# Kernel tuning notes

Hardware: AMD Instinct MI355X
Metric: run time of the kernel (lower is better)

Reference implementation:

```python
import jax, jax.numpy as jnp
import numpy as np

NBITS = 8
NUM_HEADS = 6


def _quant(x, alpha, nbits=NBITS):
    # LSQ-style fake quantization with straight-through estimator.
    qn = -(2 ** (nbits - 1))        # -128
    qp = 2 ** (nbits - 1) - 1       # 127
    s = jnp.clip(x / alpha, qn, qp)
    s = s + jax.lax.stop_gradient(jnp.round(s) - s)  # STE round
    return s * alpha


def setup_inputs() -> dict:
    key = jax.random.key(0)
    ks = jax.random.split(key, 12)
    B, N, C = 2, 2048, 384
    x = jax.random.normal(ks[0], (B, N, C), dtype=jnp.float32)
    w_qkv = jax.random.normal(ks[1], (3 * C, C), dtype=jnp.float32) * 0.02
    w_proj = jax.random.normal(ks[2], (C, C), dtype=jnp.float32) * 0.02
    b_proj = jnp.zeros((C,), dtype=jnp.float32)

    def alpha(k, lo, hi):
        return jax.random.uniform(k, (1,), dtype=jnp.float32, minval=lo, maxval=hi)

    return {
        "x": x,
        "w_qkv": w_qkv,
        "w_proj": w_proj,
        "b_proj": b_proj,
        "a_qkv_w": alpha(ks[3], 0.001, 0.005),
        "a_qkv_a": alpha(ks[4], 0.02, 0.05),
        "a_proj_w": alpha(ks[5], 0.001, 0.005),
        "a_proj_a": alpha(ks[6], 0.02, 0.05),
        "a_q": alpha(ks[7], 0.01, 0.03),
        "a_k": alpha(ks[8], 0.01, 0.03),
        "a_v": alpha(ks[9], 0.01, 0.03),
        "a_attn": alpha(ks[10], 0.01, 0.03),
        "a_attn2": alpha(ks[11], 0.005, 0.01),
    }


def reference(x, w_qkv, w_proj, b_proj, a_qkv_w, a_qkv_a, a_proj_w, a_proj_a,
              a_q, a_k, a_v, a_attn, a_attn2):
    B, N, C = x.shape
    H = NUM_HEADS
    D = C // H
    scale = D ** (-0.5)

    # quantized qkv linear (no bias)
    qkv = _quant(x, a_qkv_a) @ _quant(w_qkv, a_qkv_w).T          # [B,N,3C]
    qkv = qkv.reshape(B, N, 3, H, D).transpose(2, 0, 3, 1, 4)    # [3,B,H,N,D]
    q, k, v = qkv[0], qkv[1], qkv[2]
    q = _quant(q, a_q)
    k = _quant(k, a_k)
    v = _quant(v, a_v)

    attn = jnp.einsum("bhnd,bhmd->bhnm", q, k) * scale           # [B,H,N,N]
    attn = _quant(attn, a_attn)
    attn = jax.nn.softmax(attn, axis=-1)
    attn = _quant(attn, a_attn2)

    out = jnp.einsum("bhnm,bhmd->bhnd", attn, v)                 # [B,H,N,D]
    out = out.transpose(0, 2, 1, 3).reshape(B, N, C)

    # quantized output projection (with bias)
    out = _quant(out, a_proj_a) @ _quant(w_proj, a_proj_w).T + b_proj
    return out
```

## Files before the change

kernel.cpp:

```cpp
#include <hip/hip_runtime.h>
#include <math.h>


typedef int i32x4 __attribute__((ext_vector_type(4)));

#define MFMA_I8(a, b, c) __builtin_amdgcn_mfma_i32_16x16x64_i8(a, b, c, 0, 0, 0)

__device__ __forceinline__ float qclip(float s) {
  return fminf(fmaxf(s, -128.0f), 127.0f);
}

__global__ __launch_bounds__(256)
void quant16(const float* __restrict__ in, signed char* __restrict__ out,
             const float* __restrict__ alpha, int n16) {
  int i = blockIdx.x * 256 + threadIdx.x;
  if (i >= n16) return;
  float a = alpha[0];
  const float4* p = (const float4*)in + 4 * (size_t)i;
  union { uint4 u; signed char c[16]; } o;
#pragma unroll
  for (int u = 0; u < 4; ++u) {
    float4 v = p[u];
    o.c[4 * u + 0] = (signed char)(int)rintf(qclip(v.x / a));
    o.c[4 * u + 1] = (signed char)(int)rintf(qclip(v.y / a));
    o.c[4 * u + 2] = (signed char)(int)rintf(qclip(v.z / a));
    o.c[4 * u + 3] = (signed char)(int)rintf(qclip(v.w / a));
  }
  *(uint4*)(out + 16 * (size_t)i) = o.u;
}

__global__ __launch_bounds__(256)
void exp_table(float* __restrict__ E2, const float* __restrict__ aattn) {
  int i = blockIdx.x * 256 + threadIdx.x;
  float a = aattn[0];
  int vm = (i >> 8) - 128;
  int s = (i & 255) - 128;
  float m = a * (float)vm;
  E2[i] = expf(a * (float)s - m);
}

__global__ __launch_bounds__(256)
void gemm_qkv(const signed char* __restrict__ A, const signed char* __restrict__ W,
              signed char* __restrict__ qws, signed char* __restrict__ kws,
              signed char* __restrict__ vwsT,
              const float* __restrict__ aa, const float* __restrict__ aw,
              const float* __restrict__ aq, const float* __restrict__ ak,
              const float* __restrict__ av) {
  const int t = threadIdx.x;
  const int w = t >> 6, lane = t & 63;
  const int lm = lane & 15, quad = lane >> 4;
  const int wm = w >> 1, wn = w & 1;
  const int m0 = blockIdx.x * 128 + wm * 64;
  const int n0 = blockIdx.y * 128 + wn * 64;
  i32x4 acc[4][4] = {};
  for (int k0 = 0; k0 < 384; k0 += 64) {
    i32x4 af[4], bf[4];
#pragma unroll
    for (int mt = 0; mt < 4; ++mt)
      af[mt] = *(const i32x4*)(A + (size_t)(m0 + mt * 16 + lm) * 384 + k0 + quad * 16);
#pragma unroll
    for (int nt = 0; nt < 4; ++nt)
      bf[nt] = *(const i32x4*)(W + (size_t)(n0 + nt * 16 + lm) * 384 + k0 + quad * 16);
#pragma unroll
    for (int mt = 0; mt < 4; ++mt)
#pragma unroll
      for (int nt = 0; nt < 4; ++nt)
        acc[mt][nt] = MFMA_I8(af[mt], bf[nt], acc[mt][nt]);
  }
  const float sAB = aa[0] * aw[0];
  const float vaq = aq[0], vak = ak[0], vav = av[0];
#pragma unroll
  for (int mt = 0; mt < 4; ++mt) {
#pragma unroll
    for (int nt = 0; nt < 4; ++nt) {
      int cg = n0 + nt * 16 + lm;
      int t3 = cg / 384;
      int rem = cg - t3 * 384;
      int h = rem >> 6, d = rem & 63;
#pragma unroll
      for (int r = 0; r < 4; ++r) {
        int m = m0 + mt * 16 + quad * 4 + r;
        int bb = m >> 11, nn = m & 2047;
        int bh = bb * 6 + h;
        float val = (float)acc[mt][nt][r] * sAB;
        if (t3 == 0) {
          qws[((size_t)(bh * 2048 + nn) << 6) + d] = (signed char)(int)rintf(qclip(val / vaq));
        } else if (t3 == 1) {
          kws[((size_t)(bh * 2048 + nn) << 6) + d] = (signed char)(int)rintf(qclip(val / vak));
        } else {
          vwsT[((size_t)((bh << 6) + d) << 11) + nn] = (signed char)(int)rintf(qclip(val / vav));
        }
      }
    }
  }
}

#define TROW 2064
__global__ __launch_bounds__(256)
void attn_fused(const signed char* __restrict__ qws, const signed char* __restrict__ kws,
                const signed char* __restrict__ vwsT, const float* __restrict__ E2,
                signed char* __restrict__ ows,
                const float* __restrict__ aq, const float* __restrict__ ak,
                const float* __restrict__ aattn, const float* __restrict__ aattn2,
                const float* __restrict__ av, const float* __restrict__ apa) {
  __shared__ signed char tileS[16 * TROW];
  __shared__ float EfS[16 * 256];
  const int t = threadIdx.x;
  const int w = t >> 6, lane = t & 63;
  const int lm = lane & 15, quad = lane >> 4;
  const int i0 = blockIdx.x * 16;
  const int bh = blockIdx.y;

  const signed char* Qb = qws + ((size_t)bh << 17);
  const signed char* Kb = kws + ((size_t)bh << 17);

  i32x4 bq = *(const i32x4*)(Qb + ((size_t)(i0 + lm) << 6) + quad * 16);
  const float sc = aq[0] * ak[0] * 0.125f;
  const float ia = aattn[0];
#pragma unroll 4
  for (int ct = 0; ct < 32; ++ct) {
    int col0 = (w << 9) + ct * 16;
    i32x4 akf = *(const i32x4*)(Kb + ((size_t)(col0 + lm) << 6) + quad * 16);
    i32x4 z = {};
    i32x4 acc = MFMA_I8(akf, bq, z);
    union { unsigned int u; signed char c[4]; } pk;
#pragma unroll
    for (int r = 0; r < 4; ++r) {
      float sv = (float)acc[r] * sc;
      pk.c[r] = (signed char)(int)rintf(qclip(sv / ia));
    }
    *(unsigned int*)(tileS + lm * TROW + col0 + quad * 4) = pk.u;
  }
  __syncthreads();

  const float a2 = aattn2[0];
  unsigned int pqpack[4];
  signed char* lut8 = (signed char*)EfS;
#pragma unroll
  for (int rr = 0; rr < 4; ++rr) {
    const int row = w * 4 + rr;
    const char4* prow = (const char4*)(tileS + row * TROW);
    char4 vals[8];
    int vmax = -129;
#pragma unroll
    for (int u = 0; u < 8; ++u) {
      vals[u] = prow[lane + (u << 6)];
      vmax = max(vmax, (int)vals[u].x);
      vmax = max(vmax, (int)vals[u].y);
      vmax = max(vmax, (int)vals[u].z);
      vmax = max(vmax, (int)vals[u].w);
    }
#pragma unroll
    for (int off = 32; off > 0; off >>= 1)
      vmax = max(vmax, __shfl_xor(vmax, off, 64));
    float4 ef = *(const float4*)(E2 + (((vmax + 128) << 8) + (lane << 2)));
    *(float4*)(EfS + (row << 8) + (lane << 2)) = ef;
    const float* Er = EfS + (row << 8) + 128;
    float l = 0.0f;
#pragma unroll
    for (int u = 0; u < 8; ++u) {
      l += Er[(int)vals[u].x];
      l += Er[(int)vals[u].y];
      l += Er[(int)vals[u].z];
      l += Er[(int)vals[u].w];
    }
#pragma unroll
    for (int off = 32; off > 0; off >>= 1)
      l += __shfl_xor(l, off, 64);
    union { unsigned int u; signed char c[4]; } pk;
    pk.c[0] = (signed char)(int)rintf(qclip(ef.x / l / a2));
    pk.c[1] = (signed char)(int)rintf(qclip(ef.y / l / a2));
    pk.c[2] = (signed char)(int)rintf(qclip(ef.z / l / a2));
    pk.c[3] = (signed char)(int)rintf(qclip(ef.w / l / a2));
    pqpack[rr] = pk.u;
  }
  __syncthreads();

#pragma unroll
  for (int rr = 0; rr < 4; ++rr)
    *(unsigned int*)(lut8 + (((w * 4 + rr) << 8) + (lane << 2))) = pqpack[rr];
  __syncthreads();

  i32x4 areg[8];
  {
    const signed char* lr = lut8 + lm * 256 + 128;
    const signed char* srow = tileS + lm * TROW + (w << 9) + quad * 16;
#pragma unroll
    for (int js = 0; js < 8; ++js) {
      union { uint4 u; signed char c[16]; } sv;
      sv.u = *(const uint4*)(srow + js * 64);
      union { i32x4 v; signed char c[16]; } dv;
#pragma unroll
      for (int b = 0; b < 16; ++b) dv.c[b] = lr[(int)sv.c[b]];
      areg[js] = dv.v;
    }
  }

  const signed char* Vb = vwsT + ((size_t)bh << 17) + (w << 9);
  i32x4 acc[4] = {};
#pragma unroll
  for (int js = 0; js < 8; ++js) {
    int j0 = js * 64;
    i32x4 bf[4];
#pragma unroll
    for (int nt = 0; nt < 4; ++nt)
      bf[nt] = *(const i32x4*)(Vb + ((size_t)(nt * 16 + lm) << 11) + j0 + quad * 16);
#pragma unroll
    for (int nt = 0; nt < 4; ++nt)
      acc[nt] = MFMA_I8(areg[js], bf[nt], acc[nt]);
  }

  int* red = (int*)tileS;
  __syncthreads();
  if (w > 0) {
    int* rw = red + (w - 1) * 1088 + lane * 17;
#pragma unroll
    for (int nt = 0; nt < 4; ++nt)
#pragma unroll
      for (int r = 0; r < 4; ++r)
        rw[nt * 4 + r] = acc[nt][r];
  }
  __syncthreads();
  if (w == 0) {
    const float so = a2 * av[0];
    const float ipa = apa[0];
    int bb = bh / 6, h = bh % 6;
#pragma unroll
    for (int nt = 0; nt < 4; ++nt) {
      int d = nt * 16 + lm;
#pragma unroll
      for (int r = 0; r < 4; ++r) {
        int s = acc[nt][r] + red[lane * 17 + nt * 4 + r]
              + red[1088 + lane * 17 + nt * 4 + r]
              + red[2176 + lane * 17 + nt * 4 + r];
        int i = i0 + quad * 4 + r;
        ows[(size_t)((bb << 11) + i) * 384 + (h << 6) + d] =
            (signed char)(int)rintf(qclip((float)s * so / ipa));
      }
    }
  }
}

__global__ __launch_bounds__(256)
void gemm_proj(const signed char* __restrict__ A, const signed char* __restrict__ W,
               const float* __restrict__ bias, float* __restrict__ out,
               const float* __restrict__ apa, const float* __restrict__ apw) {
  const int t = threadIdx.x;
  const int w = t >> 6, lane = t & 63;
  const int lm = lane & 15, quad = lane >> 4;
  const int wm = w >> 1, wn = w & 1;
  const int m0 = blockIdx.x * 64 + wm * 32;
  const int n0 = blockIdx.y * 64 + wn * 32;
  i32x4 acc[2][2] = {};
  for (int k0 = 0; k0 < 384; k0 += 64) {
    i32x4 af[2], bf[2];
#pragma unroll
    for (int mt = 0; mt < 2; ++mt)
      af[mt] = *(const i32x4*)(A + (size_t)(m0 + mt * 16 + lm) * 384 + k0 + quad * 16);
#pragma unroll
    for (int nt = 0; nt < 2; ++nt)
      bf[nt] = *(const i32x4*)(W + (size_t)(n0 + nt * 16 + lm) * 384 + k0 + quad * 16);
#pragma unroll
    for (int mt = 0; mt < 2; ++mt)
#pragma unroll
      for (int nt = 0; nt < 2; ++nt)
        acc[mt][nt] = MFMA_I8(af[mt], bf[nt], acc[mt][nt]);
  }
  const float sAB = apa[0] * apw[0];
#pragma unroll
  for (int mt = 0; mt < 2; ++mt) {
#pragma unroll
    for (int nt = 0; nt < 2; ++nt) {
      int cg = n0 + nt * 16 + lm;
#pragma unroll
      for (int r = 0; r < 4; ++r) {
        int m = m0 + mt * 16 + quad * 4 + r;
        out[(size_t)m * 384 + cg] = (float)acc[mt][nt][r] * sAB + bias[cg];
      }
    }
  }
}

extern "C" void kernel_launch(void* const* d_in, const int* in_sizes, int n_in,
                              void* d_out, int out_size, void* d_ws, size_t ws_size,
                              hipStream_t stream) {
  const float* x        = (const float*)d_in[0];
  const float* w_qkv    = (const float*)d_in[1];
  const float* w_proj   = (const float*)d_in[2];
  const float* b_proj   = (const float*)d_in[3];
  const float* a_qkv_w  = (const float*)d_in[4];
  const float* a_qkv_a  = (const float*)d_in[5];
  const float* a_proj_w = (const float*)d_in[6];
  const float* a_proj_a = (const float*)d_in[7];
  const float* a_q      = (const float*)d_in[8];
  const float* a_k      = (const float*)d_in[9];
  const float* a_v      = (const float*)d_in[10];
  const float* a_attn   = (const float*)d_in[11];
  const float* a_attn2  = (const float*)d_in[12];

  char* wsb = (char*)d_ws;
  signed char* xq   = (signed char*)(wsb + 0);
  signed char* wqq  = (signed char*)(wsb + 1572864);
  signed char* wpq  = (signed char*)(wsb + 2015232);
  signed char* qws  = (signed char*)(wsb + 2162688);
  signed char* kws  = (signed char*)(wsb + 3735552);
  signed char* vwsT = (signed char*)(wsb + 5308416);
  signed char* ows  = (signed char*)(wsb + 6881280);
  float*       E2   = (float*)(wsb + 8454144);

  quant16<<<384, 256, 0, stream>>>(x, xq, a_qkv_a, 98304);
  quant16<<<108, 256, 0, stream>>>(w_qkv, wqq, a_qkv_w, 27648);
  quant16<<<36, 256, 0, stream>>>(w_proj, wpq, a_proj_w, 9216);
  exp_table<<<256, 256, 0, stream>>>(E2, a_attn);
  gemm_qkv<<<dim3(32, 9), 256, 0, stream>>>(xq, wqq, qws, kws, vwsT,
                                            a_qkv_a, a_qkv_w, a_q, a_k, a_v);
  attn_fused<<<dim3(128, 12), 256, 0, stream>>>(qws, kws, vwsT, E2, ows,
                                                a_q, a_k, a_attn, a_attn2,
                                                a_v, a_proj_a);
  gemm_proj<<<dim3(64, 6), 256, 0, stream>>>(ows, wpq, b_proj, (float*)d_out,
                                             a_proj_a, a_proj_w);
}
```

Baseline: 184.9 us.

## Merge prep kernels, use reciprocal division, and pad softmax LUT in shared memory

Combines the three quantization launches and the exp-table launch into one prep kernel, removing three launch overheads. In the attention kernel, division by the attention alpha becomes a reciprocal multiply with one Newton correction. The softmax probability LUT is now stored as padded int rows (stride 257) written directly, which drops one __syncthreads and a register staging pass and should reduce LDS bank conflicts on the gather. The int LUT gives each row its own padded stride, and the gather now reads 32-bit entries instead of bytes.

```diff
diff --git a/kernel.cpp b/kernel.cpp
--- a/kernel.cpp
+++ b/kernel.cpp
@@ -10,12 +10,15 @@
   return fminf(fmaxf(s, -128.0f), 127.0f);
 }
 
-__global__ __launch_bounds__(256)
-void quant16(const float* __restrict__ in, signed char* __restrict__ out,
-             const float* __restrict__ alpha, int n16) {
-  int i = blockIdx.x * 256 + threadIdx.x;
-  if (i >= n16) return;
-  float a = alpha[0];
+__device__ __forceinline__ float fdivn(float x, float c, float rc) {
+  float q0 = x * rc;
+  float e = fmaf(-c, q0, x);
+  return fmaf(e, rc, q0);
+}
+
+__device__ __forceinline__ void quant16_body(const float* __restrict__ in,
+                                             signed char* __restrict__ out,
+                                             float a, int i) {
   const float4* p = (const float4*)in + 4 * (size_t)i;
   union { uint4 u; signed char c[16]; } o;
 #pragma unroll
@@ -30,13 +33,30 @@
 }
 
 __global__ __launch_bounds__(256)
-void exp_table(float* __restrict__ E2, const float* __restrict__ aattn) {
-  int i = blockIdx.x * 256 + threadIdx.x;
-  float a = aattn[0];
-  int vm = (i >> 8) - 128;
-  int s = (i & 255) - 128;
-  float m = a * (float)vm;
-  E2[i] = expf(a * (float)s - m);
+void prep(const float* __restrict__ x, const float* __restrict__ wqkv,
+          const float* __restrict__ wproj,
+          signed char* __restrict__ xq, signed char* __restrict__ wqq,
+          signed char* __restrict__ wpq, float* __restrict__ E2,
+          const float* __restrict__ a_qkv_a, const float* __restrict__ a_qkv_w,
+          const float* __restrict__ a_proj_w, const float* __restrict__ aattn) {
+  const int b = blockIdx.x, t = threadIdx.x;
+  if (b < 384) {
+    int i = b * 256 + t;
+    if (i < 98304) quant16_body(x, xq, a_qkv_a[0], i);
+  } else if (b < 492) {
+    int i = (b - 384) * 256 + t;
+    if (i < 27648) quant16_body(wqkv, wqq, a_qkv_w[0], i);
+  } else if (b < 528) {
+    int i = (b - 492) * 256 + t;
+    if (i < 9216) quant16_body(wproj, wpq, a_proj_w[0], i);
+  } else {
+    int i = (b - 528) * 256 + t;
+    float a = aattn[0];
+    int vm = (i >> 8) - 128;
+    int s = (i & 255) - 128;
+    float m = a * (float)vm;
+    E2[i] = expf(a * (float)s - m);
+  }
 }
 
 __global__ __launch_bounds__(256)
@@ -104,7 +124,7 @@
                 const float* __restrict__ aattn, const float* __restrict__ aattn2,
                 const float* __restrict__ av, const float* __restrict__ apa) {
   __shared__ signed char tileS[16 * TROW];
-  __shared__ float EfS[16 * 256];
+  __shared__ float EfS[16 * 257];
   const int t = threadIdx.x;
   const int w = t >> 6, lane = t & 63;
   const int lm = lane & 15, quad = lane >> 4;
@@ -117,6 +137,7 @@
   i32x4 bq = *(const i32x4*)(Qb + ((size_t)(i0 + lm) << 6) + quad * 16);
   const float sc = aq[0] * ak[0] * 0.125f;
   const float ia = aattn[0];
+  const float ria = 1.0f / ia;
 #pragma unroll 4
   for (int ct = 0; ct < 32; ++ct) {
     int col0 = (w << 9) + ct * 16;
@@ -127,15 +148,14 @@
 #pragma unroll
     for (int r = 0; r < 4; ++r) {
       float sv = (float)acc[r] * sc;
-      pk.c[r] = (signed char)(int)rintf(qclip(sv / ia));
+      pk.c[r] = (signed char)(int)rintf(qclip(fdivn(sv, ia, ria)));
     }
     *(unsigned int*)(tileS + lm * TROW + col0 + quad * 4) = pk.u;
   }
   __syncthreads();
 
   const float a2 = aattn2[0];
-  unsigned int pqpack[4];
-  signed char* lut8 = (signed char*)EfS;
+  int* lutI = (int*)EfS;
 #pragma unroll
   for (int rr = 0; rr < 4; ++rr) {
     const int row = w * 4 + rr;
@@ -153,9 +173,13 @@
 #pragma unroll
     for (int off = 32; off > 0; off >>= 1)
       vmax = max(vmax, __shfl_xor(vmax, off, 64));
-    float4 ef = *(const float4*)(E2 + (((vmax + 128) << 8) + (lane << 2)));
-    *(float4*)(EfS + (row << 8) + (lane << 2)) = ef;
-    const float* Er = EfS + (row << 8) + 128;
+    float efu[4];
+#pragma unroll
+    for (int u = 0; u < 4; ++u) {
+      efu[u] = E2[((vmax + 128) << 8) + u * 64 + lane];
+      EfS[row * 257 + u * 64 + lane] = efu[u];
+    }
+    const float* Er = EfS + row * 257 + 128;
     float l = 0.0f;
 #pragma unroll
     for (int u = 0; u < 8; ++u) {
@@ -167,23 +191,17 @@
 #pragma unroll
     for (int off = 32; off > 0; off >>= 1)
       l += __shfl_xor(l, off, 64);
-    union { unsigned int u; signed char c[4]; } pk;
-    pk.c[0] = (signed char)(int)rintf(qclip(ef.x / l / a2));
-    pk.c[1] = (signed char)(int)rintf(qclip(ef.y / l / a2));
-    pk.c[2] = (signed char)(int)rintf(qclip(ef.z / l / a2));
-    pk.c[3] = (signed char)(int)rintf(qclip(ef.w / l / a2));
-    pqpack[rr] = pk.u;
-  }
-  __syncthreads();
-
-#pragma unroll
-  for (int rr = 0; rr < 4; ++rr)
-    *(unsigned int*)(lut8 + (((w * 4 + rr) << 8) + (lane << 2))) = pqpack[rr];
+#pragma unroll
+    for (int u = 0; u < 4; ++u) {
+      int pq = (int)(signed char)(int)rintf(qclip(efu[u] / l / a2));
+      lutI[row * 257 + u * 64 + lane] = pq;
+    }
+  }
   __syncthreads();
 
   i32x4 areg[8];
   {
-    const signed char* lr = lut8 + lm * 256 + 128;
+    const int* lr = lutI + lm * 257 + 128;
     const signed char* srow = tileS + lm * TROW + (w << 9) + quad * 16;
 #pragma unroll
     for (int js = 0; js < 8; ++js) {
@@ -191,7 +209,7 @@
       sv.u = *(const uint4*)(srow + js * 64);
       union { i32x4 v; signed char c[16]; } dv;
 #pragma unroll
-      for (int b = 0; b < 16; ++b) dv.c[b] = lr[(int)sv.c[b]];
+      for (int b = 0; b < 16; ++b) dv.c[b] = (signed char)lr[(int)sv.c[b]];
       areg[js] = dv.v;
     }
   }
@@ -308,10 +326,8 @@
   signed char* ows  = (signed char*)(wsb + 6881280);
   float*       E2   = (float*)(wsb + 8454144);
 
-  quant16<<<384, 256, 0, stream>>>(x, xq, a_qkv_a, 98304);
-  quant16<<<108, 256, 0, stream>>>(w_qkv, wqq, a_qkv_w, 27648);
-  quant16<<<36, 256, 0, stream>>>(w_proj, wpq, a_proj_w, 9216);
-  exp_table<<<256, 256, 0, stream>>>(E2, a_attn);
+  prep<<<784, 256, 0, stream>>>(x, w_qkv, w_proj, xq, wqq, wpq, E2,
+                                a_qkv_a, a_qkv_w, a_proj_w, a_attn);
   gemm_qkv<<<dim3(32, 9), 256, 0, stream>>>(xq, wqq, qws, kws, vwsT,
                                             a_qkv_a, a_qkv_w, a_q, a_k, a_v);
   attn_fused<<<dim3(128, 12), 256, 0, stream>>>(qws, kws, vwsT, E2, ows,
```

New measurement: 167.4 us. -9.5%, faster.
